# Optimization experiments

Measured on AMD Instinct MI355X. Metric: run time of the kernel, lower is better.

## Reference

```python
import jax, jax.numpy as jnp
import numpy as np
jax.config.update("jax_enable_x64", True)  # original does softmax in torch.double

B, H, S, D = 1, 16, 2048, 128

def setup_inputs() -> dict:
    key = jax.random.key(0)
    kq, kk, kv = jax.random.split(key, 3)
    return {
        "query_states": jax.random.normal(kq, (B, H, S, D), dtype=jnp.float32),
        "key_states": jax.random.normal(kk, (B, H, S, D), dtype=jnp.float32),
        "value_states": jax.random.normal(kv, (B, H, S, D), dtype=jnp.float32),
        "attention_mask": jnp.zeros((1, 1, S, S), dtype=jnp.float32),  # accepted but unused by the module
        "attention_dropout": 0,  # p=0.0 -> dropout is identity
    }

def reference(query_states, key_states, value_states, attention_mask, attention_dropout):
    head_dim = query_states.shape[-1]
    q_len = query_states.shape[-2]
    kv_len = key_states.shape[-2]
    # scores: [B,H,q,kv]
    attn = jnp.einsum("bhqd,bhkd->bhqk", query_states, key_states) / jnp.sqrt(
        jnp.asarray(head_dim, query_states.dtype))
    # causal mask: triu(ones, diagonal=1) -> mask strictly-future positions with -10000
    causal = jnp.triu(jnp.ones((q_len, kv_len), dtype=bool), k=1)
    attn = jnp.where(causal[None, None], jnp.asarray(-10000.0, attn.dtype), attn)
    # softmax in float64 (torch.double) then cast back, matching the original
    attn = jax.nn.softmax(attn.astype(jnp.float64), axis=-1).astype(query_states.dtype)
    # dropout p == attention_dropout == 0.0 -> no-op
    return jnp.einsum("bhqk,bhkd->bhqd", attn, value_states)
```

## Files before the change

### kernel.cpp

```cpp
#include <hip/hip_runtime.h>


#define NH  16
#define SEQ 2048
#define DIM 128
#define NT  64
#define SCALE 0.08838834764831845f
#define SCLOG2E 0.12751364605544427f

typedef __attribute__((ext_vector_type(8))) short    bf16x8;
typedef __attribute__((ext_vector_type(4))) float    f32x4;
typedef __attribute__((ext_vector_type(8))) unsigned short ushort8;

__device__ __forceinline__ unsigned short f2bf(float f) {
    unsigned u = __builtin_bit_cast(unsigned, f);
    u += 0x7FFFu + ((u >> 16) & 1u);
    return (unsigned short)(u >> 16);
}

__global__ void pack_kv(const float* __restrict__ K, const float* __restrict__ V,
                        unsigned short* __restrict__ Kp, unsigned short* __restrict__ Vp) {
    __shared__ float sm[32][133];
    const int t = blockIdx.x, head = blockIdx.y, tid = threadIdx.x;
    const float* __restrict__ src = blockIdx.z ? V : K;
    const size_t base = (size_t)head * SEQ * DIM + (size_t)t * 32 * DIM;
#pragma unroll
    for (int i = 0; i < 16; ++i) {
        const int idx = i * 256 + tid;
        sm[idx >> 7][idx & 127] = src[base + idx];
    }
    __syncthreads();
    if (blockIdx.z == 0) {
        ushort8* outp = reinterpret_cast<ushort8*>(Kp) + (size_t)(head * NT + t) * 512;
#pragma unroll
        for (int c = tid; c < 512; c += 256) {
            const int j = c >> 6, lane = c & 63, l15 = lane & 15, lg = lane >> 4;
            const int kl = (j >> 2) * 16 + l15, d0 = (j & 3) * 32 + lg * 8;
            ushort8 o;
#pragma unroll
            for (int e = 0; e < 8; ++e) o[e] = f2bf(sm[kl][d0 + e]);
            outp[c] = o;
        }
    } else {
        ushort8* outp = reinterpret_cast<ushort8*>(Vp) + (size_t)(head * NT + t) * 512;
#pragma unroll
        for (int c = tid; c < 512; c += 256) {
            const int db = c >> 6, lane = c & 63, l15 = lane & 15, lg = lane >> 4;
            const int d = db * 16 + l15;
            ushort8 o;
#pragma unroll
            for (int e = 0; e < 4; ++e) o[e]     = f2bf(sm[lg * 4 + e][d]);
#pragma unroll
            for (int e = 0; e < 4; ++e) o[4 + e] = f2bf(sm[16 + lg * 4 + e][d]);
            outp[c] = o;
        }
    }
}

__global__ __launch_bounds__(512, 2) void attn_main(
    const float* __restrict__ Qf, const unsigned short* __restrict__ Kp,
    const unsigned short* __restrict__ Vp, float* __restrict__ O)
{
    const int lane = threadIdx.x & 63;
    const int wid  = threadIdx.x >> 6;
    const int l15  = lane & 15;
    const int lg   = lane >> 4;
    const int bid  = blockIdx.x;
    const int head = (bid & 7) + 8 * ((bid >> 3) & 1);
    const int bx   = bid >> 4;
    const int s4   = wid & 3;
    const int lightIdx = bx * 4 + s4;
    const int qtile = (wid < 4) ? lightIdx : (127 - lightIdx);
    const int qbase = qtile * 16;
    const int nt    = qtile / 2 + 1;
    const size_t ho = (size_t)head * SEQ * DIM;

    bf16x8 qfrag[4];
    {
        const float* qrow = Qf + ho + (size_t)(qbase + l15) * DIM;
#pragma unroll
        for (int mi = 0; mi < 4; ++mi) {
            const float4 a = *reinterpret_cast<const float4*>(qrow + mi * 32 + lg * 8);
            const float4 b = *reinterpret_cast<const float4*>(qrow + mi * 32 + lg * 8 + 4);
            bf16x8 f;
            f[0]=(short)f2bf(a.x*SCLOG2E); f[1]=(short)f2bf(a.y*SCLOG2E);
            f[2]=(short)f2bf(a.z*SCLOG2E); f[3]=(short)f2bf(a.w*SCLOG2E);
            f[4]=(short)f2bf(b.x*SCLOG2E); f[5]=(short)f2bf(b.y*SCLOG2E);
            f[6]=(short)f2bf(b.z*SCLOG2E); f[7]=(short)f2bf(b.w*SCLOG2E);
            qfrag[mi] = f;
        }
    }

    f32x4 oacc[8];
#pragma unroll
    for (int i = 0; i < 8; ++i) oacc[i] = f32x4{0.f, 0.f, 0.f, 0.f};
    float l_run = 0.f;

    const bf16x8* kbase = reinterpret_cast<const bf16x8*>(Kp) + (size_t)head * NT * 512 + lane;
    const bf16x8* vbase = reinterpret_cast<const bf16x8*>(Vp) + (size_t)head * NT * 512 + lane;

    auto LOADT = [&](int T, bf16x8 (&KF)[8], bf16x8 (&VF)[8]) {
        const bf16x8* kp = kbase + (size_t)T * 512;
        const bf16x8* vp = vbase + (size_t)T * 512;
#pragma unroll
        for (int j = 0; j < 8; ++j) KF[j] = kp[j * 64];
#pragma unroll
        for (int j = 0; j < 8; ++j) VF[j] = vp[j * 64];
    };
    auto COMPUTE = [&](int T, bf16x8 (&KF)[8], bf16x8 (&VF)[8]) {
        f32x4 sT0 = f32x4{0.f,0.f,0.f,0.f}, sT1 = f32x4{0.f,0.f,0.f,0.f};
#pragma unroll
        for (int mi = 0; mi < 4; ++mi) {
            sT0 = __builtin_amdgcn_mfma_f32_16x16x32_bf16(KF[mi],     qfrag[mi], sT0, 0, 0, 0);
            sT1 = __builtin_amdgcn_mfma_f32_16x16x32_bf16(KF[4 + mi], qfrag[mi], sT1, 0, 0, 0);
        }
        float sc[8];
#pragma unroll
        for (int r = 0; r < 4; ++r) { sc[r] = sT0[r]; sc[4 + r] = sT1[r]; }
        const int kb = T * 32;
        if (kb + 31 > qbase) {
            const int qg = qbase + l15;
#pragma unroll
            for (int r = 0; r < 4; ++r) {
                if (kb + lg * 4 + r > qg)      sc[r]     = -1e30f;
                if (kb + 16 + lg * 4 + r > qg) sc[4 + r] = -1e30f;
            }
        }
        float p[8];
#pragma unroll
        for (int i = 0; i < 8; ++i) { p[i] = exp2f(sc[i]); l_run += p[i]; }
        bf16x8 pf;
#pragma unroll
        for (int i = 0; i < 8; ++i) pf[i] = (short)f2bf(p[i]);
#pragma unroll
        for (int db = 0; db < 8; ++db)
            oacc[db] = __builtin_amdgcn_mfma_f32_16x16x32_bf16(VF[db], pf, oacc[db], 0, 0, 0);
    };

    bf16x8 kA[8], vA[8], kB[8], vB[8];
    LOADT(0, kA, vA);
    for (int t = 0; t < nt; ) {
        if (t + 1 < nt) LOADT(t + 1, kB, vB);
        COMPUTE(t, kA, vA);
        ++t; if (t >= nt) break;
        if (t + 1 < nt) LOADT(t + 1, kA, vA);
        COMPUTE(t, kB, vB);
        ++t;
    }

    float lsum = l_run;
    lsum += __shfl_xor(lsum, 16);
    lsum += __shfl_xor(lsum, 32);
    const float inv = 1.f / lsum;
    float* orow = O + ho + (size_t)(qbase + l15) * DIM;
#pragma unroll
    for (int db = 0; db < 8; ++db) {
        const float4 o{oacc[db][0] * inv, oacc[db][1] * inv, oacc[db][2] * inv, oacc[db][3] * inv};
        *reinterpret_cast<float4*>(orow + db * 16 + lg * 4) = o;
    }
}

__global__ __launch_bounds__(256, 2) void attn_fb(
    const float* __restrict__ Qf, const float* __restrict__ Kf, const float* __restrict__ Vf,
    float* __restrict__ O)
{
    const int lane = threadIdx.x & 63;
    const int wid  = threadIdx.x >> 6;
    const int l15  = lane & 15;
    const int lg   = lane >> 4;
    const int head = blockIdx.y;
    const int qt   = gridDim.x - 1 - blockIdx.x;
    const int qbase = qt * 64 + wid * 16;
    const int qmax  = qbase + 15;
    const size_t ho = (size_t)head * SEQ * DIM;

    bf16x8 qfrag[4];
    const float* qrow = Qf + ho + (size_t)(qbase + l15) * DIM;
#pragma unroll
    for (int mi = 0; mi < 4; ++mi) {
        const float4 a = *reinterpret_cast<const float4*>(qrow + mi * 32 + lg * 8);
        const float4 b = *reinterpret_cast<const float4*>(qrow + mi * 32 + lg * 8 + 4);
        bf16x8 f;
        f[0]=(short)f2bf(a.x); f[1]=(short)f2bf(a.y); f[2]=(short)f2bf(a.z); f[3]=(short)f2bf(a.w);
        f[4]=(short)f2bf(b.x); f[5]=(short)f2bf(b.y); f[6]=(short)f2bf(b.z); f[7]=(short)f2bf(b.w);
        qfrag[mi] = f;
    }
    f32x4 oacc[8];
#pragma unroll
    for (int i = 0; i < 8; ++i) oacc[i] = f32x4{0.f, 0.f, 0.f, 0.f};
    float m_run = -1e38f, l_run = 0.f;
    for (int kb = 0; kb <= qmax; kb += 32) {
        f32x4 sT0 = f32x4{0.f,0.f,0.f,0.f}, sT1 = f32x4{0.f,0.f,0.f,0.f};
        const float* k0 = Kf + ho + (size_t)(kb + l15) * DIM;
        const float* k1 = k0 + 16 * DIM;
#pragma unroll
        for (int mi = 0; mi < 4; ++mi) {
            float4 a = *reinterpret_cast<const float4*>(k0 + mi * 32 + lg * 8);
            float4 b = *reinterpret_cast<const float4*>(k0 + mi * 32 + lg * 8 + 4);
            bf16x8 f;
            f[0]=(short)f2bf(a.x); f[1]=(short)f2bf(a.y); f[2]=(short)f2bf(a.z); f[3]=(short)f2bf(a.w);
            f[4]=(short)f2bf(b.x); f[5]=(short)f2bf(b.y); f[6]=(short)f2bf(b.z); f[7]=(short)f2bf(b.w);
            sT0 = __builtin_amdgcn_mfma_f32_16x16x32_bf16(f, qfrag[mi], sT0, 0, 0, 0);
            a = *reinterpret_cast<const float4*>(k1 + mi * 32 + lg * 8);
            b = *reinterpret_cast<const float4*>(k1 + mi * 32 + lg * 8 + 4);
            f[0]=(short)f2bf(a.x); f[1]=(short)f2bf(a.y); f[2]=(short)f2bf(a.z); f[3]=(short)f2bf(a.w);
            f[4]=(short)f2bf(b.x); f[5]=(short)f2bf(b.y); f[6]=(short)f2bf(b.z); f[7]=(short)f2bf(b.w);
            sT1 = __builtin_amdgcn_mfma_f32_16x16x32_bf16(f, qfrag[mi], sT1, 0, 0, 0);
        }
        float s[8];
#pragma unroll
        for (int r = 0; r < 4; ++r) { s[r] = sT0[r] * SCALE; s[4 + r] = sT1[r] * SCALE; }
        if (kb + 31 > qbase) {
            const int qg = qbase + l15;
#pragma unroll
            for (int r = 0; r < 4; ++r) {
                if (kb + lg * 4 + r > qg)      s[r]     = -1e30f;
                if (kb + 16 + lg * 4 + r > qg) s[4 + r] = -1e30f;
            }
        }
        float mt = s[0];
#pragma unroll
        for (int i = 1; i < 8; ++i) mt = fmaxf(mt, s[i]);
        mt = fmaxf(mt, __shfl_xor(mt, 16));
        mt = fmaxf(mt, __shfl_xor(mt, 32));
        const float m_new = fmaxf(m_run, mt);
        const float alpha = __expf(m_run - m_new);
        float p[8], psum = 0.f;
#pragma unroll
        for (int i = 0; i < 8; ++i) { p[i] = __expf(s[i] - m_new); psum += p[i]; }
        psum += __shfl_xor(psum, 16);
        psum += __shfl_xor(psum, 32);
        l_run = l_run * alpha + psum;
        m_run = m_new;
#pragma unroll
        for (int i = 0; i < 8; ++i) {
            oacc[i][0] *= alpha; oacc[i][1] *= alpha; oacc[i][2] *= alpha; oacc[i][3] *= alpha;
        }
        bf16x8 pf;
#pragma unroll
        for (int i = 0; i < 8; ++i) pf[i] = (short)f2bf(p[i]);
#pragma unroll
        for (int db = 0; db < 8; ++db) {
            bf16x8 vf;
#pragma unroll
            for (int e = 0; e < 8; ++e) {
                const int key = kb + 16 * (e >> 2) + lg * 4 + (e & 3);
                vf[e] = (short)f2bf(Vf[ho + (size_t)key * DIM + db * 16 + l15]);
            }
            oacc[db] = __builtin_amdgcn_mfma_f32_16x16x32_bf16(vf, pf, oacc[db], 0, 0, 0);
        }
    }
    const float inv = 1.f / l_run;
    float* orow = O + ho + (size_t)(qbase + l15) * DIM;
#pragma unroll
    for (int db = 0; db < 8; ++db) {
        const float4 o{oacc[db][0] * inv, oacc[db][1] * inv, oacc[db][2] * inv, oacc[db][3] * inv};
        *reinterpret_cast<float4*>(orow + db * 16 + lg * 4) = o;
    }
}

extern "C" void kernel_launch(void* const* d_in, const int* in_sizes, int n_in,
                              void* d_out, int out_size, void* d_ws, size_t ws_size,
                              hipStream_t stream) {
    const float* Q = (const float*)d_in[0];
    const float* K = (const float*)d_in[1];
    const float* V = (const float*)d_in[2];
    float* O = (float*)d_out;

    const size_t ELEMS = (size_t)NH * SEQ * DIM;
    const size_t NEED  = 2 * ELEMS * sizeof(unsigned short);

    if (ws_size >= NEED) {
        unsigned short* Kp = (unsigned short*)d_ws;
        unsigned short* Vp = Kp + ELEMS;
        pack_kv<<<dim3(NT, NH, 2), dim3(256), 0, stream>>>(K, V, Kp, Vp);
        attn_main<<<dim3(256), dim3(512), 0, stream>>>(Q, Kp, Vp, O);
    } else {
        attn_fb<<<dim3(SEQ / 64, NH), dim3(256), 0, stream>>>(Q, K, V, O);
    }
}
```

Before: 146.2 us.

## Share K/V tiles across waves via double-buffered LDS staging

Each wave used to load its own K/V fragments from global memory. Now the four waves of a 256-thread block cooperatively stage each K/V tile into a double-buffered LDS array and read their fragments from there, synchronising with __syncthreads per tile. The grid is remapped to 512 blocks, each covering a contiguous 64-row query slab, with heavy slabs scheduled first instead of pairing light and heavy tiles inside one block. This aims to cut redundant global and L2 traffic, at the cost of a block barrier on every tile and lost load balance within a block, since waves that finish early still wait at the barriers.

Result: slower. 211.3 us (+44.6%).

```diff
diff --git a/kernel.cpp b/kernel.cpp
--- a/kernel.cpp
+++ b/kernel.cpp
@@ -57,22 +57,23 @@
     }
 }
 
-__global__ __launch_bounds__(512, 2) void attn_main(
+__global__ __launch_bounds__(256, 2) void attn_main(
     const float* __restrict__ Qf, const unsigned short* __restrict__ Kp,
     const unsigned short* __restrict__ Vp, float* __restrict__ O)
 {
+    __shared__ uint4 lds[2][16][64];
     const int lane = threadIdx.x & 63;
     const int wid  = threadIdx.x >> 6;
     const int l15  = lane & 15;
     const int lg   = lane >> 4;
     const int bid  = blockIdx.x;
-    const int head = (bid & 7) + 8 * ((bid >> 3) & 1);
-    const int bx   = bid >> 4;
-    const int s4   = wid & 3;
-    const int lightIdx = bx * 4 + s4;
-    const int qtile = (wid < 4) ? lightIdx : (127 - lightIdx);
-    const int qbase = qtile * 16;
-    const int nt    = qtile / 2 + 1;
+    const int xcd  = bid & 7;
+    const int j    = bid >> 3;
+    const int head = xcd * 2 + (j & 1);
+    const int slab = 31 - (j >> 1);
+    const int qbase = slab * 64 + wid * 16;
+    const int ntb   = 2 * slab + 2;
+    const int ntw   = (qbase + 15) / 32 + 1;
     const size_t ho = (size_t)head * SEQ * DIM;
 
     bf16x8 qfrag[4];
@@ -96,23 +97,35 @@
     for (int i = 0; i < 8; ++i) oacc[i] = f32x4{0.f, 0.f, 0.f, 0.f};
     float l_run = 0.f;
 
-    const bf16x8* kbase = reinterpret_cast<const bf16x8*>(Kp) + (size_t)head * NT * 512 + lane;
-    const bf16x8* vbase = reinterpret_cast<const bf16x8*>(Vp) + (size_t)head * NT * 512 + lane;
-
-    auto LOADT = [&](int T, bf16x8 (&KF)[8], bf16x8 (&VF)[8]) {
-        const bf16x8* kp = kbase + (size_t)T * 512;
-        const bf16x8* vp = vbase + (size_t)T * 512;
-#pragma unroll
-        for (int j = 0; j < 8; ++j) KF[j] = kp[j * 64];
-#pragma unroll
-        for (int j = 0; j < 8; ++j) VF[j] = vp[j * 64];
+    const uint4* ktile = reinterpret_cast<const uint4*>(Kp) + (size_t)head * NT * 512;
+    const uint4* vtile = reinterpret_cast<const uint4*>(Vp) + (size_t)head * NT * 512;
+
+    auto STAGE_LOAD = [&](int T, uint4 (&st)[4]) {
+#pragma unroll
+        for (int i = 0; i < 4; ++i) {
+            const int slot = wid * 4 + i;
+            const uint4* src = (slot < 8)
+                ? (ktile + (size_t)T * 512 + slot * 64 + lane)
+                : (vtile + (size_t)T * 512 + (slot - 8) * 64 + lane);
+            st[i] = *src;
+        }
     };
-    auto COMPUTE = [&](int T, bf16x8 (&KF)[8], bf16x8 (&VF)[8]) {
+    auto STAGE_WRITE = [&](int b, uint4 (&st)[4]) {
+#pragma unroll
+        for (int i = 0; i < 4; ++i) lds[b][wid * 4 + i][lane] = st[i];
+    };
+    auto COMPUTE = [&](int T, int b) {
+        bf16x8 kf[8], vf[8];
+#pragma unroll
+        for (int s = 0; s < 8; ++s) kf[s] = *reinterpret_cast<const bf16x8*>(&lds[b][s][lane]);
+#pragma unroll
+        for (int s = 0; s < 8; ++s) vf[s] = *reinterpret_cast<const bf16x8*>(&lds[b][8 + s][lane]);
+
         f32x4 sT0 = f32x4{0.f,0.f,0.f,0.f}, sT1 = f32x4{0.f,0.f,0.f,0.f};
 #pragma unroll
         for (int mi = 0; mi < 4; ++mi) {
-            sT0 = __builtin_amdgcn_mfma_f32_16x16x32_bf16(KF[mi],     qfrag[mi], sT0, 0, 0, 0);
-            sT1 = __builtin_amdgcn_mfma_f32_16x16x32_bf16(KF[4 + mi], qfrag[mi], sT1, 0, 0, 0);
+            sT0 = __builtin_amdgcn_mfma_f32_16x16x32_bf16(kf[mi],     qfrag[mi], sT0, 0, 0, 0);
+            sT1 = __builtin_amdgcn_mfma_f32_16x16x32_bf16(kf[4 + mi], qfrag[mi], sT1, 0, 0, 0);
         }
         float sc[8];
 #pragma unroll
@@ -134,18 +147,24 @@
         for (int i = 0; i < 8; ++i) pf[i] = (short)f2bf(p[i]);
 #pragma unroll
         for (int db = 0; db < 8; ++db)
-            oacc[db] = __builtin_amdgcn_mfma_f32_16x16x32_bf16(VF[db], pf, oacc[db], 0, 0, 0);
+            oacc[db] = __builtin_amdgcn_mfma_f32_16x16x32_bf16(vf[db], pf, oacc[db], 0, 0, 0);
     };
 
-    bf16x8 kA[8], vA[8], kB[8], vB[8];
-    LOADT(0, kA, vA);
-    for (int t = 0; t < nt; ) {
-        if (t + 1 < nt) LOADT(t + 1, kB, vB);
-        COMPUTE(t, kA, vA);
-        ++t; if (t >= nt) break;
-        if (t + 1 < nt) LOADT(t + 1, kA, vA);
-        COMPUTE(t, kB, vB);
-        ++t;
+    uint4 st[4];
+    STAGE_LOAD(0, st);
+    STAGE_WRITE(0, st);
+    __syncthreads();
+
+    int cur = 0;
+    for (int t = 0; t < ntb; ++t) {
+        const bool more = (t + 1 < ntb);
+        if (more) STAGE_LOAD(t + 1, st);
+        if (t < ntw) COMPUTE(t, cur);
+        if (more) {
+            STAGE_WRITE(cur ^ 1, st);
+            __syncthreads();
+            cur ^= 1;
+        }
     }
 
     float lsum = l_run;
@@ -274,7 +293,7 @@
         unsigned short* Kp = (unsigned short*)d_ws;
         unsigned short* Vp = Kp + ELEMS;
         pack_kv<<<dim3(NT, NH, 2), dim3(256), 0, stream>>>(K, V, Kp, Vp);
-        attn_main<<<dim3(256), dim3(512), 0, stream>>>(Q, Kp, Vp, O);
+        attn_main<<<dim3(512), dim3(256), 0, stream>>>(Q, Kp, Vp, O);
     } else {
         attn_fb<<<dim3(SEQ / 64, NH), dim3(256), 0, stream>>>(Q, K, V, O);
     }
```
